# Optimization experiments

Hardware: AMD Instinct MI355X
Metric: run time of the kernel (lower is better)

The kernel has to match this reference:

```python
import jax, jax.numpy as jnp
import numpy as np

B, L, E, H = 128, 256, 256, 512


def setup_inputs() -> dict:
    key = jax.random.key(0)
    ks = jax.random.split(key, 16)
    s = 0.02
    return {
        "embedded_inputs": jax.random.normal(ks[0], (B, L, E), jnp.float32),
        "decoder_input": jax.random.normal(ks[1], (B, E), jnp.float32),
        "dec_h": jax.random.normal(ks[2], (B, H), jnp.float32),
        "dec_c": jax.random.normal(ks[3], (B, H), jnp.float32),
        "context": jax.random.normal(ks[4], (B, L, H), jnp.float32),
        # Decoder params
        "W_i2h": jax.random.normal(ks[5], (4 * H, E), jnp.float32) * s,
        "b_i2h": jnp.zeros((4 * H,), jnp.float32),
        "W_h2h": jax.random.normal(ks[6], (4 * H, H), jnp.float32) * s,
        "b_h2h": jnp.zeros((4 * H,), jnp.float32),
        "W_out": jax.random.normal(ks[7], (H, 2 * H), jnp.float32) * s,
        "b_out": jnp.zeros((H,), jnp.float32),
        # Attention params
        "W_inp": jax.random.normal(ks[8], (H, H), jnp.float32) * s,
        "b_inp": jnp.zeros((H,), jnp.float32),
        "W_ctx": jax.random.normal(ks[9], (H, H), jnp.float32) * s,  # Conv1d(k=1) kernel squeezed
        "b_ctx": jnp.zeros((H,), jnp.float32),
        "V": jax.random.uniform(ks[10], (H,), jnp.float32, -1.0, 1.0),
    }


def reference(embedded_inputs, decoder_input, dec_h, dec_c, context,
              W_i2h, b_i2h, W_h2h, b_h2h, W_out, b_out,
              W_inp, b_inp, W_ctx, b_ctx, V):
    # Precompute projected context: Conv1d(k=1) == per-position linear. ctx: [B, H, L]
    ctx = jnp.einsum("blh,gh->bgl", context, W_ctx) + b_ctx[None, :, None]
    seq_len = embedded_inputs.shape[1]

    def step(carry, _):
        x, h, c, mask = carry
        gates = x @ W_i2h.T + b_i2h + h @ W_h2h.T + b_h2h
        i, f, g, o = jnp.split(gates, 4, axis=1)
        c_t = jax.nn.sigmoid(f) * c + jax.nn.sigmoid(i) * jnp.tanh(g)
        h_t = jax.nn.sigmoid(o) * jnp.tanh(c_t)
        # attention
        inp = h_t @ W_inp.T + b_inp                              # [B, H]
        scores = jnp.einsum("h,bhl->bl", V, jnp.tanh(inp[:, :, None] + ctx))
        att = jnp.where(mask == 0, -jnp.inf, scores)
        alpha = jax.nn.softmax(att, axis=-1)                     # [B, L]
        hidden = jnp.einsum("bhl,bl->bh", ctx, alpha)
        h_new = jnp.tanh(jnp.concatenate([hidden, h_t], axis=1) @ W_out.T + b_out)
        # pointer selection
        idx = jnp.argmax(alpha * mask, axis=1)                   # [B]
        one_hot = jax.nn.one_hot(idx, seq_len, dtype=mask.dtype)
        mask_new = mask * (1.0 - one_hot)
        next_x = jnp.take_along_axis(embedded_inputs, idx[:, None, None], axis=1)[:, 0, :]
        return (next_x, h_new, c_t, mask_new), (alpha, idx)

    mask0 = jnp.ones((embedded_inputs.shape[0], seq_len), jnp.float32)
    (x_f, h_f, c_f, _), (alphas, ptrs) = jax.lax.scan(
        step, (decoder_input, dec_h, dec_c, mask0), None, length=seq_len)
    outputs = jnp.transpose(alphas, (1, 0, 2))   # [B, L, L]
    pointers = jnp.transpose(ptrs, (1, 0))       # [B, L]
    return outputs, pointers, h_f, c_f
```

## Files before the change

### kernel.cpp

```cpp
#include <hip/hip_runtime.h>

#define B 128
#define L 256
#define E 256
#define H 512
#define NBLK 256
#define NTHR 512

typedef float f4 __attribute__((ext_vector_type(4)));

#define WS_CTX 0u
#define WS_HT  16777216u
#define WS_HH  16908288u
#define WS_HID 17039360u
#define WS_INP 17170432u
#define WS_XT  17301504u
#define WS_FLG 17367040u

#define FLG_PG 0u
#define FLG_PI 4096u
#define FLG_PA 8192u
#define FLG_PH 12288u

#define OUT_ALPHA 0u
#define OUT_PTR   8388608u
#define OUT_H     8421376u
#define OUT_C     8486912u

#define L2E 1.4426950408889634f

__device__ __forceinline__ float fast_rcp(float x) { return __builtin_amdgcn_rcpf(x); }

__device__ __forceinline__ float ftanh(float x) {
  float e = exp2f(x * (2.0f * L2E));
  return 1.0f - 2.0f * fast_rcp(e + 1.0f);
}
__device__ __forceinline__ float fsig(float x) {
  float e = exp2f(-x * L2E);
  return fast_rcp(1.0f + e);
}

#define CLD1(v0, p0)                                                          \
  asm volatile("global_load_dwordx4 %0, %1, off sc0 sc1\n\t"                  \
               "s_waitcnt vmcnt(0)"                                           \
               : "=&v"(v0) : "v"(p0) : "memory")

#define CLD2(va, pa)                                                          \
  asm volatile("global_load_dwordx4 %0, %2, off sc0 sc1\n\t"                  \
               "global_load_dwordx4 %1, %3, off sc0 sc1\n\t"                  \
               "s_waitcnt vmcnt(0)"                                           \
               : "=&v"(va[0]), "=&v"(va[1])                                   \
               : "v"(pa[0]), "v"(pa[1]) : "memory")

#define CLD4(va, pa)                                                          \
  asm volatile("global_load_dwordx4 %0, %4, off sc0 sc1\n\t"                  \
               "global_load_dwordx4 %1, %5, off sc0 sc1\n\t"                  \
               "global_load_dwordx4 %2, %6, off sc0 sc1\n\t"                  \
               "global_load_dwordx4 %3, %7, off sc0 sc1\n\t"                  \
               "s_waitcnt vmcnt(0)"                                           \
               : "=&v"(va[0]), "=&v"(va[1]), "=&v"(va[2]), "=&v"(va[3])       \
               : "v"(pa[0]), "v"(pa[1]), "v"(pa[2]), "v"(pa[3]) : "memory")

#define CLD6(va, pa)                                                          \
  asm volatile("global_load_dwordx4 %0, %6, off sc0 sc1\n\t"                  \
               "global_load_dwordx4 %1, %7, off sc0 sc1\n\t"                  \
               "global_load_dwordx4 %2, %8, off sc0 sc1\n\t"                  \
               "global_load_dwordx4 %3, %9, off sc0 sc1\n\t"                  \
               "global_load_dwordx4 %4, %10, off sc0 sc1\n\t"                 \
               "global_load_dwordx4 %5, %11, off sc0 sc1\n\t"                 \
               "s_waitcnt vmcnt(0)"                                           \
               : "=&v"(va[0]), "=&v"(va[1]), "=&v"(va[2]), "=&v"(va[3]),      \
                 "=&v"(va[4]), "=&v"(va[5])                                   \
               : "v"(pa[0]), "v"(pa[1]), "v"(pa[2]), "v"(pa[3]),              \
                 "v"(pa[4]), "v"(pa[5]) : "memory")

#define CST4_1(p0, v0)                                                        \
  asm volatile("global_store_dwordx4 %0, %1, off sc0 sc1\n\t"                 \
               "s_waitcnt expcnt(0)"                                          \
               :: "v"(p0), "v"(v0) : "memory")

__device__ __forceinline__ void wait_ge(const unsigned* fp, bool act, unsigned tgt) {
  for (;;) {
    unsigned f = tgt;
    if (act) {
      asm volatile("global_load_dword %0, %1, off sc0 sc1\n\ts_waitcnt vmcnt(0)"
                   : "=&v"(f) : "v"(fp) : "memory");
    }
    if (__all(f >= tgt)) break;
    __builtin_amdgcn_s_sleep(1);
  }
}

#define PUBLISH(ARROFF) do {                                                  \
    asm volatile("s_waitcnt vmcnt(0) lgkmcnt(0) expcnt(0)" ::: "memory");     \
    __syncthreads();                                                          \
    if (t == 0) {                                                             \
      unsigned* fp_ = flags + (ARROFF) + (unsigned)bid * 16u;                 \
      unsigned v_ = (unsigned)(step + 1);                                     \
      asm volatile("global_store_dword %0, %1, off sc0 sc1"                   \
                   :: "v"(fp_), "v"(v_) : "memory");                          \
    }                                                                         \
  } while (0)

__global__ __launch_bounds__(256) void k_ctx(const float* __restrict__ context,
                                             const float* __restrict__ Wc,
                                             const float* __restrict__ bc,
                                             float* __restrict__ ws) {
  __shared__ float a_lds[64][33];
  __shared__ float b_lds[32][68];
  int t = threadIdx.x;
  int m0 = blockIdx.x * 64;
  int n0 = blockIdx.y * 64;
  int tx = t & 15, ty = t >> 4;
  float acc[4][4] = {};
  for (int kc = 0; kc < 16; ++kc) {
    int k0 = kc * 32;
    __syncthreads();
#pragma unroll
    for (int i = 0; i < 2; ++i) {
      int f40 = t + i * 256;
      int mm = f40 >> 3;
      int k4 = (f40 & 7) * 4;
      float4 v = *(const float4*)&context[(size_t)(m0 + mm) * H + k0 + k4];
      a_lds[mm][k4] = v.x; a_lds[mm][k4 + 1] = v.y; a_lds[mm][k4 + 2] = v.z; a_lds[mm][k4 + 3] = v.w;
    }
#pragma unroll
    for (int i = 0; i < 2; ++i) {
      int f40 = t + i * 256;
      int nn = f40 >> 3;
      int k4 = (f40 & 7) * 4;
      float4 v = *(const float4*)&Wc[(size_t)(n0 + nn) * H + k0 + k4];
      b_lds[k4][nn] = v.x; b_lds[k4 + 1][nn] = v.y; b_lds[k4 + 2][nn] = v.z; b_lds[k4 + 3][nn] = v.w;
    }
    __syncthreads();
#pragma unroll
    for (int kk = 0; kk < 32; ++kk) {
      float4 bv = *(const float4*)&b_lds[kk][tx * 4];
      float a0 = a_lds[ty * 4 + 0][kk], a1 = a_lds[ty * 4 + 1][kk];
      float a2 = a_lds[ty * 4 + 2][kk], a3 = a_lds[ty * 4 + 3][kk];
      acc[0][0] += a0 * bv.x; acc[0][1] += a0 * bv.y; acc[0][2] += a0 * bv.z; acc[0][3] += a0 * bv.w;
      acc[1][0] += a1 * bv.x; acc[1][1] += a1 * bv.y; acc[1][2] += a1 * bv.z; acc[1][3] += a1 * bv.w;
      acc[2][0] += a2 * bv.x; acc[2][1] += a2 * bv.y; acc[2][2] += a2 * bv.z; acc[2][3] += a2 * bv.w;
      acc[3][0] += a3 * bv.x; acc[3][1] += a3 * bv.y; acc[3][2] += a3 * bv.z; acc[3][3] += a3 * bv.w;
    }
  }
  float b0v = bc[n0 + tx * 4], b1v = bc[n0 + tx * 4 + 1], b2v = bc[n0 + tx * 4 + 2], b3v = bc[n0 + tx * 4 + 3];
#pragma unroll
  for (int i = 0; i < 4; ++i) {
    size_t o = WS_CTX + (size_t)(m0 + ty * 4 + i) * H + n0 + tx * 4;
    float4 v; v.x = acc[i][0] + b0v; v.y = acc[i][1] + b1v; v.z = acc[i][2] + b2v; v.w = acc[i][3] + b3v;
    *(float4*)&ws[o] = v;
  }
}

__global__ __launch_bounds__(256) void k_init(const float* __restrict__ dec_h,
                                              const float* __restrict__ dec_in,
                                              float* __restrict__ ws) {
  int flat = blockIdx.x * 256 + threadIdx.x;
  if (flat < 65536) {
    ws[WS_HH + flat] = dec_h[flat];
  } else if (flat < 98304) {
    ws[WS_XT + (flat - 65536)] = dec_in[flat - 65536];
  } else if (flat < 114688) {
    ((unsigned*)(ws + WS_FLG))[flat - 98304] = 0u;
  }
}

__global__ __launch_bounds__(512, 1) void k_main(
    const float* __restrict__ Wi2h, const float* __restrict__ bi2h,
    const float* __restrict__ Wh2h, const float* __restrict__ bh2h,
    const float* __restrict__ Wout, const float* __restrict__ bout,
    const float* __restrict__ Winp, const float* __restrict__ binp,
    const float* __restrict__ Vv,   const float* __restrict__ emb,
    const float* __restrict__ dec_c,
    float* __restrict__ ws,         float* __restrict__ out) {
  __shared__ float s_act[13504];
  __shared__ float s_maskP[256];
  __shared__ float s_mw[8], s_dw[8];
  __shared__ float s_red[4];
  __shared__ int   s_redi[4];
  __shared__ int   s_wc[4], s_wb[4];
  __shared__ int   s_mi, s_cnt;

  unsigned* flags = (unsigned*)(ws + WS_FLG);
  const int bid = blockIdx.x;
  const int t = threadIdx.x;
  const int wv = t >> 6, ln = t & 63;

  float creg = 0.f;

  if (bid < 128 && t < 256) s_maskP[t] = 1.0f;
  __syncthreads();

  for (int step = 0; step < L; ++step) {
    const unsigned pr = (unsigned)(step & 1);
    float* HTc  = ws + WS_HT  + pr * 65536u;
    float* HHr  = ws + WS_HH  + pr * 65536u;
    float* HHw  = ws + WS_HH  + (pr ^ 1u) * 65536u;
    float* HIDc = ws + WS_HID + pr * 65536u;
    float* INPc = ws + WS_INP + pr * 65536u;
    float* XTr  = ws + WS_XT  + pr * 32768u;
    float* XTw  = ws + WS_XT  + (pr ^ 1u) * 32768u;

    {
      const int jt = (bid & 7) * 4 + ((bid >> 3) & 3);
      const int bt = bid >> 5;
      const int u0 = jt * 16, b0 = bt * 16;
      if (step > 0) {
        if (wv == 0) {
          const unsigned* fp = flags;
          bool act = false;
          if (ln < 32) { fp = flags + FLG_PH + ((unsigned)bt * 32u + (unsigned)ln) * 16u; act = true; }
          else if (ln < 48) { fp = flags + FLG_PA + ((unsigned)bt * 16u + (unsigned)(ln - 32)) * 16u; act = true; }
          wait_ge(fp, act, (unsigned)step);
        }
        __syncthreads();
      }
      float* sact = s_act;
      float* sg   = s_act + 12352;
      f4 va[6]; const float* pa[6]; int sb[6], sq[6];
#pragma unroll
      for (int it = 0; it < 6; ++it) {
        unsigned c = (unsigned)(t + it * 512);
        int bl = (int)(c / 192u);
        int kq = (int)(c - (unsigned)bl * 192u);
        int kg = kq * 4;
        sb[it] = bl; sq[it] = kq;
        pa[it] = (kg < 256) ? XTr + (size_t)(b0 + bl) * 256 + kg
                            : HHr + (size_t)(b0 + bl) * 512 + (kg - 256);
      }
      CLD6(va, pa);
      __builtin_amdgcn_sched_barrier(0);
#pragma unroll
      for (int it = 0; it < 6; ++it) *(f4*)&sact[sb[it] * 772 + sq[it] * 4] = va[it];
      __syncthreads();

      const int jj = t >> 4, bb = t & 15;
      const int g = jj >> 3, up = (jj & 7) * 2;
      const int r0 = g * 512 + u0 + up;
      float a0 = 0.f, a1 = 0.f;
      {
        const float* w0 = Wi2h + (size_t)r0 * 256;
        const float* w1 = w0 + 256;
        const float* sa = sact + bb * 772;
#pragma unroll 8
        for (int k4 = 0; k4 < 64; ++k4) {
          float4 x = *(const float4*)&sa[k4 * 4];
          float4 p = *(const float4*)&w0[k4 * 4];
          float4 q = *(const float4*)&w1[k4 * 4];
          a0 += p.x * x.x + p.y * x.y + p.z * x.z + p.w * x.w;
          a1 += q.x * x.x + q.y * x.y + q.z * x.z + q.w * x.w;
        }
        const float* v0 = Wh2h + (size_t)r0 * 512;
        const float* v1 = v0 + 512;
        const float* shh = sa + 256;
#pragma unroll 8
        for (int k4 = 0; k4 < 128; ++k4) {
          float4 x = *(const float4*)&shh[k4 * 4];
          float4 p = *(const float4*)&v0[k4 * 4];
          float4 q = *(const float4*)&v1[k4 * 4];
          a0 += p.x * x.x + p.y * x.y + p.z * x.z + p.w * x.w;
          a1 += q.x * x.x + q.y * x.y + q.z * x.z + q.w * x.w;
        }
      }
      sg[(g * 16 + up) * 17 + bb]     = a0;
      sg[(g * 16 + up + 1) * 17 + bb] = a1;
      __syncthreads();
      if (t < 256) {
        const int uu = t >> 4, b2 = t & 15;
        const int j0 = u0 + uu;
        float si_ = sg[(     uu) * 17 + b2] + bi2h[       j0] + bh2h[       j0];
        float sf_ = sg[(16 + uu) * 17 + b2] + bi2h[ 512 + j0] + bh2h[ 512 + j0];
        float sg_ = sg[(32 + uu) * 17 + b2] + bi2h[1024 + j0] + bh2h[1024 + j0];
        float so_ = sg[(48 + uu) * 17 + b2] + bi2h[1536 + j0] + bh2h[1536 + j0];
        if (step == 0) creg = dec_c[(size_t)(b0 + b2) * 512 + j0];
        float cn = fsig(sf_) * creg + fsig(si_) * ftanh(sg_);
        creg = cn;
        float htv = fsig(so_) * ftanh(cn);
        s_act[b2 * 17 + uu] = htv;
        if (step == L - 1) out[OUT_C + (size_t)(b0 + b2) * 512 + j0] = cn;
      }
      __syncthreads();
      if (t < 64) {
        const int b2 = t >> 2, q = t & 3;
        f4 hv;
        hv[0] = s_act[b2 * 17 + q * 4 + 0];
        hv[1] = s_act[b2 * 17 + q * 4 + 1];
        hv[2] = s_act[b2 * 17 + q * 4 + 2];
        hv[3] = s_act[b2 * 17 + q * 4 + 3];
        float* hp = HTc + (size_t)(b0 + b2) * 512 + u0 + q * 4;
        CST4_1(hp, hv);
      }
      PUBLISH(FLG_PG);
    }

    {
      const int gt = (bid & 7) * 2 + ((bid >> 3) & 1);
      const int bt = bid >> 4;
      const int g0 = gt * 32, b0 = bt * 8;
      if (wv == 0)
        wait_ge(flags + FLG_PG + ((unsigned)(bid >> 5) * 32u + (unsigned)ln) * 16u,
                ln < 32, (unsigned)(step + 1));
      __syncthreads();
      float* si = s_act;
      float* stmp = s_act + 4128;
      f4 va[2]; const float* pa[2];
#pragma unroll
      for (int it = 0; it < 2; ++it) {
        int c = t + it * 512;
        int bl = c >> 7, kq = c & 127;
        pa[it] = HTc + (size_t)(b0 + bl) * 512 + kq * 4;
      }
      CLD2(va, pa);
      __builtin_amdgcn_sched_barrier(0);
#pragma unroll
      for (int it = 0; it < 2; ++it) {
        int c = t + it * 512;
        int bl = c >> 7, kq = c & 127;
        *(f4*)&si[bl * 516 + kq * 4] = va[it];
      }
      __syncthreads();
      if (t < 256) {
        const int gl = t >> 3, bb = t & 7;
        const float* w = Winp + (size_t)(g0 + gl) * 512;
        const float* sa = si + bb * 516;
        float acc = 0.f;
#pragma unroll 8
        for (int k4 = 0; k4 < 128; ++k4) {
          float4 ww = *(const float4*)&w[k4 * 4];
          float4 xx = *(const float4*)&sa[k4 * 4];
          acc += ww.x * xx.x + ww.y * xx.y + ww.z * xx.z + ww.w * xx.w;
        }
        stmp[bb * 33 + gl] = acc + binp[g0 + gl];
      }
      __syncthreads();
      if (t < 64) {
        const int bb = t >> 3, q = t & 7;
        f4 v;
        v[0] = stmp[bb * 33 + q * 4 + 0];
        v[1] = stmp[bb * 33 + q * 4 + 1];
        v[2] = stmp[bb * 33 + q * 4 + 2];
        v[3] = stmp[bb * 33 + q * 4 + 3];
        float* p = INPc + (size_t)(b0 + bb) * 512 + g0 + q * 4;
        CST4_1(p, v);
      }
      PUBLISH(FLG_PI);
    }

    if (bid < 128) {
      const int b = bid;
      float* s_inp  = s_act;
      float* s_sc   = s_act + 512;
      int*   s_li   = (int*)(s_act + 768);
      float* s_hidp = s_act + 1024;
      float* s_out  = s_act + 5120;
      bool validl = (t < 256) && (s_maskP[t] != 0.f);
      unsigned long long bal = __ballot(validl);
      if (t < 256 && (t & 63) == 0) s_wc[t >> 6] = (int)__popcll(bal);
      __syncthreads();
      if (t == 0) {
        int base = 0;
#pragma unroll
        for (int i = 0; i < 4; ++i) { s_wb[i] = base; base += s_wc[i]; }
        s_cnt = base;
      }
      __syncthreads();
      if (validl) {
        int idx = s_wb[t >> 6] + (int)__popcll(bal & ((1ull << (t & 63)) - 1ull));
        s_li[idx] = t;
      }
      __syncthreads();
      const int cnt = s_cnt;
      const int d0 = ln * 8;
      f4 cur0a, cur0b, cur1a, cur1b, cur2a, cur2b, cur3a, cur3b;
      int l0i, l1i, l2i, l3i;
      const int base0 = wv * 4;
      {
        int s0 = base0, s1 = base0 + 1, s2 = base0 + 2, s3 = base0 + 3;
        int a = (s0 < cnt) ? s_li[s0] : 0;  l0i = (s0 < cnt) ? a : -1;
        int bb2 = (s1 < cnt) ? s_li[s1] : 0; l1i = (s1 < cnt) ? bb2 : -1;
        int c = (s2 < cnt) ? s_li[s2] : 0;  l2i = (s2 < cnt) ? c : -1;
        int d = (s3 < cnt) ? s_li[s3] : 0;  l3i = (s3 < cnt) ? d : -1;
        const f4* p0 = (const f4*)(ws + WS_CTX + ((size_t)(b * 256 + a) * 512) + d0);
        const f4* p1 = (const f4*)(ws + WS_CTX + ((size_t)(b * 256 + bb2) * 512) + d0);
        const f4* p2 = (const f4*)(ws + WS_CTX + ((size_t)(b * 256 + c) * 512) + d0);
        const f4* p3 = (const f4*)(ws + WS_CTX + ((size_t)(b * 256 + d) * 512) + d0);
        cur0a = __builtin_nontemporal_load(p0); cur0b = __builtin_nontemporal_load(p0 + 1);
        cur1a = __builtin_nontemporal_load(p1); cur1b = __builtin_nontemporal_load(p1 + 1);
        cur2a = __builtin_nontemporal_load(p2); cur2b = __builtin_nontemporal_load(p2 + 1);
        cur3a = __builtin_nontemporal_load(p3); cur3b = __builtin_nontemporal_load(p3 + 1);
      }
      if (wv == 0)
        wait_ge(flags + FLG_PI + ((unsigned)(b >> 3) * 16u + (unsigned)ln) * 16u,
                ln < 16, (unsigned)(step + 1));
      __syncthreads();
      if (t < 128) {
        f4 v;
        const float* p = INPc + (size_t)b * 512 + t * 4;
        CLD1(v, p);
        *(f4*)&s_inp[t * 4] = v;
      }
      __syncthreads();
      float inp8[8], v8[8];
#pragma unroll
      for (int i = 0; i < 8; ++i) { inp8[i] = s_inp[d0 + i]; v8[i] = Vv[d0 + i]; }
      float m = -INFINITY, den = 0.f;
      float hid[8] = {0, 0, 0, 0, 0, 0, 0, 0};
      for (int base = base0; base < cnt; base += 32) {
        f4 n0a, n0b, n1a, n1b, n2a, n2b, n3a, n3b;
        int nl0, nl1, nl2, nl3;
        {
          int s0 = base + 32, s1 = base + 33, s2 = base + 34, s3 = base + 35;
          int a = (s0 < cnt) ? s_li[s0] : 0;  nl0 = (s0 < cnt) ? a : -1;
          int bb2 = (s1 < cnt) ? s_li[s1] : 0; nl1 = (s1 < cnt) ? bb2 : -1;
          int c = (s2 < cnt) ? s_li[s2] : 0;  nl2 = (s2 < cnt) ? c : -1;
          int d = (s3 < cnt) ? s_li[s3] : 0;  nl3 = (s3 < cnt) ? d : -1;
          const f4* p0 = (const f4*)(ws + WS_CTX + ((size_t)(b * 256 + a) * 512) + d0);
          const f4* p1 = (const f4*)(ws + WS_CTX + ((size_t)(b * 256 + bb2) * 512) + d0);
          const f4* p2 = (const f4*)(ws + WS_CTX + ((size_t)(b * 256 + c) * 512) + d0);
          const f4* p3 = (const f4*)(ws + WS_CTX + ((size_t)(b * 256 + d) * 512) + d0);
          n0a = __builtin_nontemporal_load(p0); n0b = __builtin_nontemporal_load(p0 + 1);
          n1a = __builtin_nontemporal_load(p1); n1b = __builtin_nontemporal_load(p1 + 1);
          n2a = __builtin_nontemporal_load(p2); n2b = __builtin_nontemporal_load(p2 + 1);
          n3a = __builtin_nontemporal_load(p3); n3b = __builtin_nontemporal_load(p3 + 1);
        }
        float sv0, sv1, sv2, sv3;
        {
          float part = v8[0] * ftanh(inp8[0] + cur0a[0]) + v8[1] * ftanh(inp8[1] + cur0a[1])
                     + v8[2] * ftanh(inp8[2] + cur0a[2]) + v8[3] * ftanh(inp8[3] + cur0a[3])
                     + v8[4] * ftanh(inp8[4] + cur0b[0]) + v8[5] * ftanh(inp8[5] + cur0b[1])
                     + v8[6] * ftanh(inp8[6] + cur0b[2]) + v8[7] * ftanh(inp8[7] + cur0b[3]);
#pragma unroll
          for (int off = 32; off > 0; off >>= 1) part += __shfl_xor(part, off);
          if (l0i >= 0 && ln == 0) s_sc[l0i] = part;
          sv0 = (l0i >= 0) ? part : -INFINITY;
        }
        {
          float part = v8[0] * ftanh(inp8[0] + cur1a[0]) + v8[1] * ftanh(inp8[1] + cur1a[1])
                     + v8[2] * ftanh(inp8[2] + cur1a[2]) + v8[3] * ftanh(inp8[3] + cur1a[3])
                     + v8[4] * ftanh(inp8[4] + cur1b[0]) + v8[5] * ftanh(inp8[5] + cur1b[1])
                     + v8[6] * ftanh(inp8[6] + cur1b[2]) + v8[7] * ftanh(inp8[7] + cur1b[3]);
#pragma unroll
          for (int off = 32; off > 0; off >>= 1) part += __shfl_xor(part, off);
          if (l1i >= 0 && ln == 0) s_sc[l1i] = part;
          sv1 = (l1i >= 0) ? part : -INFINITY;
        }
        {
          float part = v8[0] * ftanh(inp8[0] + cur2a[0]) + v8[1] * ftanh(inp8[1] + cur2a[1])
                     + v8[2] * ftanh(inp8[2] + cur2a[2]) + v8[3] * ftanh(inp8[3] + cur2a[3])
                     + v8[4] * ftanh(inp8[4] + cur2b[0]) + v8[5] * ftanh(inp8[5] + cur2b[1])
                     + v8[6] * ftanh(inp8[6] + cur2b[2]) + v8[7] * ftanh(inp8[7] + cur2b[3]);
#pragma unroll
          for (int off = 32; off > 0; off >>= 1) part += __shfl_xor(part, off);
          if (l2i >= 0 && ln == 0) s_sc[l2i] = part;
          sv2 = (l2i >= 0) ? part : -INFINITY;
        }
        {
          float part = v8[0] * ftanh(inp8[0] + cur3a[0]) + v8[1] * ftanh(inp8[1] + cur3a[1])
                     + v8[2] * ftanh(inp8[2] + cur3a[2]) + v8[3] * ftanh(inp8[3] + cur3a[3])
                     + v8[4] * ftanh(inp8[4] + cur3b[0]) + v8[5] * ftanh(inp8[5] + cur3b[1])
                     + v8[6] * ftanh(inp8[6] + cur3b[2]) + v8[7] * ftanh(inp8[7] + cur3b[3]);
#pragma unroll
          for (int off = 32; off > 0; off >>= 1) part += __shfl_xor(part, off);
          if (l3i >= 0 && ln == 0) s_sc[l3i] = part;
          sv3 = (l3i >= 0) ? part : -INFINITY;
        }
        float mn = fmaxf(m, fmaxf(fmaxf(sv0, sv1), fmaxf(sv2, sv3)));
        float scale = exp2f((m - mn) * L2E);
        float e0 = exp2f((sv0 - mn) * L2E);
        float e1 = exp2f((sv1 - mn) * L2E);
        float e2 = exp2f((sv2 - mn) * L2E);
        float e3 = exp2f((sv3 - mn) * L2E);
        den = den * scale + ((e0 + e1) + (e2 + e3));
        hid[0] = hid[0] * scale + e0 * cur0a[0] + e1 * cur1a[0] + e2 * cur2a[0] + e3 * cur3a[0];
        hid[1] = hid[1] * scale + e0 * cur0a[1] + e1 * cur1a[1] + e2 * cur2a[1] + e3 * cur3a[1];
        hid[2] = hid[2] * scale + e0 * cur0a[2] + e1 * cur1a[2] + e2 * cur2a[2] + e3 * cur3a[2];
        hid[3] = hid[3] * scale + e0 * cur0a[3] + e1 * cur1a[3] + e2 * cur2a[3] + e3 * cur3a[3];
        hid[4] = hid[4] * scale + e0 * cur0b[0] + e1 * cur1b[0] + e2 * cur2b[0] + e3 * cur3b[0];
        hid[5] = hid[5] * scale + e0 * cur0b[1] + e1 * cur1b[1] + e2 * cur2b[1] + e3 * cur3b[1];
        hid[6] = hid[6] * scale + e0 * cur0b[2] + e1 * cur1b[2] + e2 * cur2b[2] + e3 * cur3b[2];
        hid[7] = hid[7] * scale + e0 * cur0b[3] + e1 * cur1b[3] + e2 * cur2b[3] + e3 * cur3b[3];
        m = mn;
        cur0a = n0a; cur0b = n0b; cur1a = n1a; cur1b = n1b;
        cur2a = n2a; cur2b = n2b; cur3a = n3a; cur3b = n3b;
        l0i = nl0; l1i = nl1; l2i = nl2; l3i = nl3;
      }
      if (ln == 0) { s_mw[wv] = m; s_dw[wv] = den; }
      __syncthreads();
      float M = s_mw[0];
#pragma unroll
      for (int w = 1; w < 8; ++w) M = fmaxf(M, s_mw[w]);
      float D = 0.f;
#pragma unroll
      for (int w = 0; w < 8; ++w) D += s_dw[w] * exp2f((s_mw[w] - M) * L2E);
      float fac = exp2f((m - M) * L2E);
#pragma unroll
      for (int i = 0; i < 8; ++i) s_hidp[wv * 512 + d0 + i] = hid[i] * fac;
      __syncthreads();
      const float rD = 1.0f / D;
      {
        float hs = 0.f;
#pragma unroll
        for (int w = 0; w < 8; ++w) hs += s_hidp[w * 512 + t];
        s_out[t] = hs * rD;
      }
      float sc = 0.f; bool valid = false;
      if (t < 256) {
        valid = (s_maskP[t] != 0.f);
        sc = s_sc[t];
        float alpha = valid ? exp2f((sc - M) * L2E) * rD : 0.f;
        out[OUT_ALPHA + ((size_t)b * 256 + step) * 256 + t] = alpha;
        float bs = valid ? sc : -INFINITY;
        int bi = t;
#pragma unroll
        for (int off = 32; off > 0; off >>= 1) {
          float os = __shfl_down(bs, off);
          int oi = __shfl_down(bi, off);
          if (os > bs || (os == bs && oi < bi)) { bs = os; bi = oi; }
        }
        if ((t & 63) == 0) { s_red[t >> 6] = bs; s_redi[t >> 6] = bi; }
      }
      __syncthreads();
      if (t == 0) {
        float mm = s_red[0]; int mi = s_redi[0];
#pragma unroll
        for (int w = 1; w < 4; ++w) {
          if (s_red[w] > mm || (s_red[w] == mm && s_redi[w] < mi)) { mm = s_red[w]; mi = s_redi[w]; }
        }
        s_mi = mi;
      }
      __syncthreads();
      const int mi = s_mi;
      if (t < 128) {
        f4 hv = *(const f4*)&s_out[t * 4];
        float* hp = HIDc + (size_t)b * 512 + t * 4;
        CST4_1(hp, hv);
      }
      if (t < 64) {
        float4 xv = *(const float4*)&emb[((size_t)b * 256 + mi) * 256 + t * 4];
        f4 xq; xq[0] = xv.x; xq[1] = xv.y; xq[2] = xv.z; xq[3] = xv.w;
        float* xp = XTw + (size_t)b * 256 + t * 4;
        CST4_1(xp, xq);
      }
      if (t == 0) {
        out[OUT_PTR + (size_t)b * 256 + step] = (float)mi;
        s_maskP[mi] = 0.f;
      }
      PUBLISH(FLG_PA);
    }

    {
      const int rt = (bid & 7) * 2 + ((bid >> 3) & 1);
      const int bt = bid >> 4;
      const int r0 = rt * 32, b0 = bt * 8;
      float* sh = s_act;
      float* stmp = s_act + 8224;
      f4 va[4]; const float* pa[4];
#pragma unroll
      for (int it = 0; it < 4; ++it) {
        int c = t + it * 512;
        int bl = c >> 8, kq = c & 255;
        int kg = kq * 4;
        pa[it] = (kg < 512) ? HIDc + (size_t)(b0 + bl) * 512 + kg
                            : HTc + (size_t)(b0 + bl) * 512 + (kg - 512);
      }
      const bool isHT = (t & 128);
      if (wv == 0)
        wait_ge(flags + FLG_PG + ((unsigned)(bid >> 5) * 32u + (unsigned)ln) * 16u,
                ln < 32, (unsigned)(step + 1));
      __syncthreads();
      if (isHT) {
        CLD4(va, pa);
        __builtin_amdgcn_sched_barrier(0);
#pragma unroll
        for (int it = 0; it < 4; ++it) {
          int c = t + it * 512;
          int bl = c >> 8, kq = c & 255;
          *(f4*)&sh[bl * 1028 + kq * 4] = va[it];
        }
      }
      if (wv == 0)
        wait_ge(flags + FLG_PA + ((unsigned)b0 + (unsigned)ln) * 16u,
                ln < 8, (unsigned)(step + 1));
      __syncthreads();
      if (!isHT) {
        CLD4(va, pa);
        __builtin_amdgcn_sched_barrier(0);
#pragma unroll
        for (int it = 0; it < 4; ++it) {
          int c = t + it * 512;
          int bl = c >> 8, kq = c & 255;
          *(f4*)&sh[bl * 1028 + kq * 4] = va[it];
        }
      }
      __syncthreads();
      if (t < 256) {
        const int rl = t >> 3, bb = t & 7;
        const float* w = Wout + (size_t)(r0 + rl) * 1024;
        const float* sa = sh + bb * 1028;
        float acc = 0.f;
#pragma unroll 8
        for (int k4 = 0; k4 < 256; ++k4) {
          float4 ww = *(const float4*)&w[k4 * 4];
          float4 xx = *(const float4*)&sa[k4 * 4];
          acc += ww.x * xx.x + ww.y * xx.y + ww.z * xx.z + ww.w * xx.w;
        }
        float h = ftanh(acc + bout[r0 + rl]);
        stmp[bb * 33 + rl] = h;
        if (step == L - 1) out[OUT_H + (size_t)(b0 + bb) * 512 + r0 + rl] = h;
      }
      __syncthreads();
      if (t < 64) {
        const int bb = t >> 3, q = t & 7;
        f4 v;
        v[0] = stmp[bb * 33 + q * 4 + 0];
        v[1] = stmp[bb * 33 + q * 4 + 1];
        v[2] = stmp[bb * 33 + q * 4 + 2];
        v[3] = stmp[bb * 33 + q * 4 + 3];
        float* p = HHw + (size_t)(b0 + bb) * 512 + r0 + q * 4;
        CST4_1(p, v);
      }
      PUBLISH(FLG_PH);
    }
  }
}

extern "C" void kernel_launch(void* const* d_in, const int* in_sizes, int n_in,
                              void* d_out, int out_size, void* d_ws, size_t ws_size,
                              hipStream_t stream) {
  (void)in_sizes; (void)n_in; (void)out_size; (void)ws_size;
  const float* emb    = (const float*)d_in[0];
  const float* dec_in = (const float*)d_in[1];
  const float* dec_h  = (const float*)d_in[2];
  const float* dec_c  = (const float*)d_in[3];
  const float* ctx_in = (const float*)d_in[4];
  const float* W_i2h  = (const float*)d_in[5];
  const float* b_i2h  = (const float*)d_in[6];
  const float* W_h2h  = (const float*)d_in[7];
  const float* b_h2h  = (const float*)d_in[8];
  const float* W_out  = (const float*)d_in[9];
  const float* b_out  = (const float*)d_in[10];
  const float* W_inp  = (const float*)d_in[11];
  const float* b_inp  = (const float*)d_in[12];
  const float* W_ctx  = (const float*)d_in[13];
  const float* b_ctx  = (const float*)d_in[14];
  const float* Vv     = (const float*)d_in[15];
  float* out = (float*)d_out;
  float* ws  = (float*)d_ws;

  k_ctx<<<dim3(512, 8), 256, 0, stream>>>(ctx_in, W_ctx, b_ctx, ws);
  k_init<<<448, 256, 0, stream>>>(dec_h, dec_in, ws);
  k_main<<<NBLK, NTHR, 0, stream>>>(W_i2h, b_i2h, W_h2h, b_h2h, W_out, b_out,
                                    W_inp, b_inp, Vv, emb, dec_c, ws, out);
}
```

Before: 17.17 ms.

## Double persistent block count and halve per-block batch tiles in recurrent kernel

Doubles the persistent grid from 256 to 512 blocks, halving the batch tile each block handles in the gate, inp-projection and output phases. The flag arrays and their wait patterns are remapped so the new tile partitioning still finds its producers, and the shared buffer shrinks so up to four blocks can share a CU. This spreads the per-step weight streaming across more CUs to cut latency per step. In exchange it adds more cross-block flag polling and synchronisation per step. The output phase also merges its two staged waits into one, which gives up the earlier overlap of loading ht before the attention result is ready.

```diff
diff --git a/kernel.cpp b/kernel.cpp
--- a/kernel.cpp
+++ b/kernel.cpp
@@ -4,7 +4,7 @@
 #define L 256
 #define E 256
 #define H 512
-#define NBLK 256
+#define NBLK 512
 #define NTHR 512
 
 typedef float f4 __attribute__((ext_vector_type(4)));
@@ -18,9 +18,9 @@
 #define WS_FLG 17367040u
 
 #define FLG_PG 0u
-#define FLG_PI 4096u
-#define FLG_PA 8192u
-#define FLG_PH 12288u
+#define FLG_PI 8192u
+#define FLG_PA 16384u
+#define FLG_PH 24576u
 
 #define OUT_ALPHA 0u
 #define OUT_PTR   8388608u
@@ -52,27 +52,13 @@
                : "=&v"(va[0]), "=&v"(va[1])                                   \
                : "v"(pa[0]), "v"(pa[1]) : "memory")
 
-#define CLD4(va, pa)                                                          \
-  asm volatile("global_load_dwordx4 %0, %4, off sc0 sc1\n\t"                  \
-               "global_load_dwordx4 %1, %5, off sc0 sc1\n\t"                  \
-               "global_load_dwordx4 %2, %6, off sc0 sc1\n\t"                  \
-               "global_load_dwordx4 %3, %7, off sc0 sc1\n\t"                  \
+#define CLD3(va, pa)                                                          \
+  asm volatile("global_load_dwordx4 %0, %3, off sc0 sc1\n\t"                  \
+               "global_load_dwordx4 %1, %4, off sc0 sc1\n\t"                  \
+               "global_load_dwordx4 %2, %5, off sc0 sc1\n\t"                  \
                "s_waitcnt vmcnt(0)"                                           \
-               : "=&v"(va[0]), "=&v"(va[1]), "=&v"(va[2]), "=&v"(va[3])       \
-               : "v"(pa[0]), "v"(pa[1]), "v"(pa[2]), "v"(pa[3]) : "memory")
-
-#define CLD6(va, pa)                                                          \
-  asm volatile("global_load_dwordx4 %0, %6, off sc0 sc1\n\t"                  \
-               "global_load_dwordx4 %1, %7, off sc0 sc1\n\t"                  \
-               "global_load_dwordx4 %2, %8, off sc0 sc1\n\t"                  \
-               "global_load_dwordx4 %3, %9, off sc0 sc1\n\t"                  \
-               "global_load_dwordx4 %4, %10, off sc0 sc1\n\t"                 \
-               "global_load_dwordx4 %5, %11, off sc0 sc1\n\t"                 \
-               "s_waitcnt vmcnt(0)"                                           \
-               : "=&v"(va[0]), "=&v"(va[1]), "=&v"(va[2]), "=&v"(va[3]),      \
-                 "=&v"(va[4]), "=&v"(va[5])                                   \
-               : "v"(pa[0]), "v"(pa[1]), "v"(pa[2]), "v"(pa[3]),              \
-                 "v"(pa[4]), "v"(pa[5]) : "memory")
+               : "=&v"(va[0]), "=&v"(va[1]), "=&v"(va[2])                     \
+               : "v"(pa[0]), "v"(pa[1]), "v"(pa[2]) : "memory")
 
 #define CST4_1(p0, v0)                                                        \
   asm volatile("global_store_dwordx4 %0, %1, off sc0 sc1\n\t"                 \
@@ -87,7 +73,7 @@
                    : "=&v"(f) : "v"(fp) : "memory");
     }
     if (__all(f >= tgt)) break;
-    __builtin_amdgcn_s_sleep(1);
+    __builtin_amdgcn_s_sleep(2);
   }
 }
 
@@ -161,12 +147,12 @@
     ws[WS_HH + flat] = dec_h[flat];
   } else if (flat < 98304) {
     ws[WS_XT + (flat - 65536)] = dec_in[flat - 65536];
-  } else if (flat < 114688) {
+  } else if (flat < 131072) {
     ((unsigned*)(ws + WS_FLG))[flat - 98304] = 0u;
   }
 }
 
-__global__ __launch_bounds__(512, 1) void k_main(
+__global__ __launch_bounds__(512, 4) void k_main(
     const float* __restrict__ Wi2h, const float* __restrict__ bi2h,
     const float* __restrict__ Wh2h, const float* __restrict__ bh2h,
     const float* __restrict__ Wout, const float* __restrict__ bout,
@@ -174,7 +160,7 @@
     const float* __restrict__ Vv,   const float* __restrict__ emb,
     const float* __restrict__ dec_c,
     float* __restrict__ ws,         float* __restrict__ out) {
-  __shared__ float s_act[13504];
+  __shared__ float s_act[6912];
   __shared__ float s_maskP[256];
   __shared__ float s_mw[8], s_dw[8];
   __shared__ float s_red[4];
@@ -205,22 +191,29 @@
     {
       const int jt = (bid & 7) * 4 + ((bid >> 3) & 3);
       const int bt = bid >> 5;
-      const int u0 = jt * 16, b0 = bt * 16;
+      const int u0 = jt * 16, b0 = bt * 8;
       if (step > 0) {
         if (wv == 0) {
           const unsigned* fp = flags;
           bool act = false;
-          if (ln < 32) { fp = flags + FLG_PH + ((unsigned)bt * 32u + (unsigned)ln) * 16u; act = true; }
-          else if (ln < 48) { fp = flags + FLG_PA + ((unsigned)bt * 16u + (unsigned)(ln - 32)) * 16u; act = true; }
+          if (ln < 32) {
+            int btPH = bt * 2 + (ln >> 4);
+            int rt = ln & 15;
+            fp = flags + FLG_PH + (unsigned)(btPH * 16 + ((rt & 1) << 3) + (rt >> 1)) * 16u;
+            act = true;
+          } else if (ln < 40) {
+            fp = flags + FLG_PA + (unsigned)(b0 + (ln - 32)) * 16u;
+            act = true;
+          }
           wait_ge(fp, act, (unsigned)step);
         }
         __syncthreads();
       }
       float* sact = s_act;
-      float* sg   = s_act + 12352;
-      f4 va[6]; const float* pa[6]; int sb[6], sq[6];
-#pragma unroll
-      for (int it = 0; it < 6; ++it) {
+      float* sg   = s_act + 6176;
+      f4 va[3]; const float* pa[3]; int sb[3], sq[3];
+#pragma unroll
+      for (int it = 0; it < 3; ++it) {
         unsigned c = (unsigned)(t + it * 512);
         int bl = (int)(c / 192u);
         int kq = (int)(c - (unsigned)bl * 192u);
@@ -229,59 +222,52 @@
         pa[it] = (kg < 256) ? XTr + (size_t)(b0 + bl) * 256 + kg
                             : HHr + (size_t)(b0 + bl) * 512 + (kg - 256);
       }
-      CLD6(va, pa);
+      CLD3(va, pa);
       __builtin_amdgcn_sched_barrier(0);
 #pragma unroll
-      for (int it = 0; it < 6; ++it) *(f4*)&sact[sb[it] * 772 + sq[it] * 4] = va[it];
-      __syncthreads();
-
-      const int jj = t >> 4, bb = t & 15;
-      const int g = jj >> 3, up = (jj & 7) * 2;
-      const int r0 = g * 512 + u0 + up;
-      float a0 = 0.f, a1 = 0.f;
+      for (int it = 0; it < 3; ++it) *(f4*)&sact[sb[it] * 772 + sq[it] * 4] = va[it];
+      __syncthreads();
+
+      const int row = t >> 3, bb = t & 7;
+      const int g = row >> 4, uu = row & 15;
+      const int r = g * 512 + u0 + uu;
+      float a0 = 0.f;
       {
-        const float* w0 = Wi2h + (size_t)r0 * 256;
-        const float* w1 = w0 + 256;
+        const float* w0 = Wi2h + (size_t)r * 256;
         const float* sa = sact + bb * 772;
 #pragma unroll 8
         for (int k4 = 0; k4 < 64; ++k4) {
           float4 x = *(const float4*)&sa[k4 * 4];
           float4 p = *(const float4*)&w0[k4 * 4];
-          float4 q = *(const float4*)&w1[k4 * 4];
           a0 += p.x * x.x + p.y * x.y + p.z * x.z + p.w * x.w;
-          a1 += q.x * x.x + q.y * x.y + q.z * x.z + q.w * x.w;
-        }
-        const float* v0 = Wh2h + (size_t)r0 * 512;
-        const float* v1 = v0 + 512;
+        }
+        const float* v0 = Wh2h + (size_t)r * 512;
         const float* shh = sa + 256;
 #pragma unroll 8
         for (int k4 = 0; k4 < 128; ++k4) {
           float4 x = *(const float4*)&shh[k4 * 4];
           float4 p = *(const float4*)&v0[k4 * 4];
-          float4 q = *(const float4*)&v1[k4 * 4];
           a0 += p.x * x.x + p.y * x.y + p.z * x.z + p.w * x.w;
-          a1 += q.x * x.x + q.y * x.y + q.z * x.z + q.w * x.w;
-        }
-      }
-      sg[(g * 16 + up) * 17 + bb]     = a0;
-      sg[(g * 16 + up + 1) * 17 + bb] = a1;
-      __syncthreads();
-      if (t < 256) {
-        const int uu = t >> 4, b2 = t & 15;
-        const int j0 = u0 + uu;
-        float si_ = sg[(     uu) * 17 + b2] + bi2h[       j0] + bh2h[       j0];
-        float sf_ = sg[(16 + uu) * 17 + b2] + bi2h[ 512 + j0] + bh2h[ 512 + j0];
-        float sg_ = sg[(32 + uu) * 17 + b2] + bi2h[1024 + j0] + bh2h[1024 + j0];
-        float so_ = sg[(48 + uu) * 17 + b2] + bi2h[1536 + j0] + bh2h[1536 + j0];
+        }
+      }
+      sg[row * 9 + bb] = a0;
+      __syncthreads();
+      if (t < 128) {
+        const int uu2 = t >> 3, b2 = t & 7;
+        const int j0 = u0 + uu2;
+        float si_ = sg[(     uu2) * 9 + b2] + bi2h[       j0] + bh2h[       j0];
+        float sf_ = sg[(16 + uu2) * 9 + b2] + bi2h[ 512 + j0] + bh2h[ 512 + j0];
+        float sg_ = sg[(32 + uu2) * 9 + b2] + bi2h[1024 + j0] + bh2h[1024 + j0];
+        float so_ = sg[(48 + uu2) * 9 + b2] + bi2h[1536 + j0] + bh2h[1536 + j0];
         if (step == 0) creg = dec_c[(size_t)(b0 + b2) * 512 + j0];
         float cn = fsig(sf_) * creg + fsig(si_) * ftanh(sg_);
         creg = cn;
         float htv = fsig(so_) * ftanh(cn);
-        s_act[b2 * 17 + uu] = htv;
+        s_act[b2 * 17 + uu2] = htv;
         if (step == L - 1) out[OUT_C + (size_t)(b0 + b2) * 512 + j0] = cn;
       }
       __syncthreads();
-      if (t < 64) {
+      if (t < 32) {
         const int b2 = t >> 2, q = t & 3;
         f4 hv;
         hv[0] = s_act[b2 * 17 + q * 4 + 0];
@@ -296,32 +282,32 @@
 
     {
       const int gt = (bid & 7) * 2 + ((bid >> 3) & 1);
-      const int bt = bid >> 4;
-      const int g0 = gt * 32, b0 = bt * 8;
-      if (wv == 0)
-        wait_ge(flags + FLG_PG + ((unsigned)(bid >> 5) * 32u + (unsigned)ln) * 16u,
-                ln < 32, (unsigned)(step + 1));
+      const int btPI = bid >> 4;
+      const int g0 = gt * 32, b0 = btPI * 4;
+      if (wv == 0) {
+        const unsigned* fp = flags;
+        bool act = false;
+        if (ln < 32) {
+          int jt = ln;
+          fp = flags + FLG_PG + (unsigned)((btPI >> 1) * 32 + ((jt & 3) << 3) + (jt >> 2)) * 16u;
+          act = true;
+        }
+        wait_ge(fp, act, (unsigned)(step + 1));
+      }
       __syncthreads();
       float* si = s_act;
-      float* stmp = s_act + 4128;
-      f4 va[2]; const float* pa[2];
-#pragma unroll
-      for (int it = 0; it < 2; ++it) {
-        int c = t + it * 512;
-        int bl = c >> 7, kq = c & 127;
-        pa[it] = HTc + (size_t)(b0 + bl) * 512 + kq * 4;
-      }
-      CLD2(va, pa);
-      __builtin_amdgcn_sched_barrier(0);
-#pragma unroll
-      for (int it = 0; it < 2; ++it) {
-        int c = t + it * 512;
-        int bl = c >> 7, kq = c & 127;
-        *(f4*)&si[bl * 516 + kq * 4] = va[it];
-      }
-      __syncthreads();
-      if (t < 256) {
-        const int gl = t >> 3, bb = t & 7;
+      float* stmp = s_act + 2064;
+      f4 v0;
+      {
+        int bl = t >> 7, kq = t & 127;
+        const float* p = HTc + (size_t)(b0 + bl) * 512 + kq * 4;
+        CLD1(v0, p);
+        __builtin_amdgcn_sched_barrier(0);
+        *(f4*)&si[bl * 516 + kq * 4] = v0;
+      }
+      __syncthreads();
+      if (t < 128) {
+        const int gl = t >> 2, bb = t & 3;
         const float* w = Winp + (size_t)(g0 + gl) * 512;
         const float* sa = si + bb * 516;
         float acc = 0.f;
@@ -334,7 +320,7 @@
         stmp[bb * 33 + gl] = acc + binp[g0 + gl];
       }
       __syncthreads();
-      if (t < 64) {
+      if (t < 32) {
         const int bb = t >> 3, q = t & 7;
         f4 v;
         v[0] = stmp[bb * 33 + q * 4 + 0];
@@ -390,9 +376,16 @@
         cur2a = __builtin_nontemporal_load(p2); cur2b = __builtin_nontemporal_load(p2 + 1);
         cur3a = __builtin_nontemporal_load(p3); cur3b = __builtin_nontemporal_load(p3 + 1);
       }
-      if (wv == 0)
-        wait_ge(flags + FLG_PI + ((unsigned)(b >> 3) * 16u + (unsigned)ln) * 16u,
-                ln < 16, (unsigned)(step + 1));
+      if (wv == 0) {
+        const unsigned* fp = flags;
+        bool act = false;
+        if (ln < 16) {
+          int gt = ln;
+          fp = flags + FLG_PI + (unsigned)((b >> 2) * 16 + ((gt & 1) << 3) + (gt >> 1)) * 16u;
+          act = true;
+        }
+        wait_ge(fp, act, (unsigned)(step + 1));
+      }
       __syncthreads();
       if (t < 128) {
         f4 v;
@@ -551,51 +544,44 @@
 
     {
       const int rt = (bid & 7) * 2 + ((bid >> 3) & 1);
-      const int bt = bid >> 4;
-      const int r0 = rt * 32, b0 = bt * 8;
+      const int btPH = bid >> 4;
+      const int r0 = rt * 32, b0 = btPH * 4;
+      if (wv == 0) {
+        const unsigned* fp = flags;
+        bool act = false;
+        if (ln < 32) {
+          int jt = ln;
+          fp = flags + FLG_PG + (unsigned)((btPH >> 1) * 32 + ((jt & 3) << 3) + (jt >> 2)) * 16u;
+          act = true;
+        } else if (ln < 36) {
+          fp = flags + FLG_PA + (unsigned)(b0 + (ln - 32)) * 16u;
+          act = true;
+        }
+        wait_ge(fp, act, (unsigned)(step + 1));
+      }
+      __syncthreads();
       float* sh = s_act;
-      float* stmp = s_act + 8224;
-      f4 va[4]; const float* pa[4];
-#pragma unroll
-      for (int it = 0; it < 4; ++it) {
+      float* stmp = s_act + 4112;
+      f4 va[2]; const float* pa[2];
+#pragma unroll
+      for (int it = 0; it < 2; ++it) {
         int c = t + it * 512;
         int bl = c >> 8, kq = c & 255;
         int kg = kq * 4;
         pa[it] = (kg < 512) ? HIDc + (size_t)(b0 + bl) * 512 + kg
                             : HTc + (size_t)(b0 + bl) * 512 + (kg - 512);
       }
-      const bool isHT = (t & 128);
-      if (wv == 0)
-        wait_ge(flags + FLG_PG + ((unsigned)(bid >> 5) * 32u + (unsigned)ln) * 16u,
-                ln < 32, (unsigned)(step + 1));
-      __syncthreads();
-      if (isHT) {
-        CLD4(va, pa);
-        __builtin_amdgcn_sched_barrier(0);
-#pragma unroll
-        for (int it = 0; it < 4; ++it) {
-          int c = t + it * 512;
-          int bl = c >> 8, kq = c & 255;
-          *(f4*)&sh[bl * 1028 + kq * 4] = va[it];
-        }
-      }
-      if (wv == 0)
-        wait_ge(flags + FLG_PA + ((unsigned)b0 + (unsigned)ln) * 16u,
-                ln < 8, (unsigned)(step + 1));
-      __syncthreads();
-      if (!isHT) {
-        CLD4(va, pa);
-        __builtin_amdgcn_sched_barrier(0);
-#pragma unroll
-        for (int it = 0; it < 4; ++it) {
-          int c = t + it * 512;
-          int bl = c >> 8, kq = c & 255;
-          *(f4*)&sh[bl * 1028 + kq * 4] = va[it];
-        }
-      }
-      __syncthreads();
-      if (t < 256) {
-        const int rl = t >> 3, bb = t & 7;
+      CLD2(va, pa);
+      __builtin_amdgcn_sched_barrier(0);
+#pragma unroll
+      for (int it = 0; it < 2; ++it) {
+        int c = t + it * 512;
+        int bl = c >> 8, kq = c & 255;
+        *(f4*)&sh[bl * 1028 + kq * 4] = va[it];
+      }
+      __syncthreads();
+      if (t < 128) {
+        const int rl = t >> 2, bb = t & 3;
         const float* w = Wout + (size_t)(r0 + rl) * 1024;
         const float* sa = sh + bb * 1028;
         float acc = 0.f;
@@ -610,7 +596,7 @@
         if (step == L - 1) out[OUT_H + (size_t)(b0 + bb) * 512 + r0 + rl] = h;
       }
       __syncthreads();
-      if (t < 64) {
+      if (t < 32) {
         const int bb = t >> 3, q = t & 7;
         f4 v;
         v[0] = stmp[bb * 33 + q * 4 + 0];
@@ -649,7 +635,7 @@
   float* ws  = (float*)d_ws;
 
   k_ctx<<<dim3(512, 8), 256, 0, stream>>>(ctx_in, W_ctx, b_ctx, ws);
-  k_init<<<448, 256, 0, stream>>>(dec_h, dec_in, ws);
+  k_init<<<512, 256, 0, stream>>>(dec_h, dec_in, ws);
   k_main<<<NBLK, NTHR, 0, stream>>>(W_i2h, b_i2h, W_h2h, b_h2h, W_out, b_out,
                                     W_inp, b_inp, Vv, emb, dec_c, ws, out);
 }
```

After: 23.87 ms. +39.0%, slower.
